# Optimization experiments

Measured on AMD Instinct MI355X. Metric: run time of the kernel, lower is better.

Reference implementation:

```python
import jax, jax.numpy as jnp
import numpy as np

BATCH = 16384
MODEL_DIM = 768
SAE_HIDDEN = 16384
K = 3


def setup_inputs() -> dict:
    key = jax.random.key(0)
    k1, k2, k3, k4, k5 = jax.random.split(key, 5)
    scale_enc = 1.0 / np.sqrt(MODEL_DIM)
    scale_dec = 1.0 / np.sqrt(SAE_HIDDEN)
    return {
        "model_activations": jax.random.normal(k1, (BATCH, MODEL_DIM), jnp.float32),
        "W_enc": jax.random.normal(k2, (SAE_HIDDEN, MODEL_DIM), jnp.float32) * scale_enc,
        "b_enc": jax.random.normal(k3, (SAE_HIDDEN,), jnp.float32) * scale_enc,
        "W_dec": jax.random.normal(k4, (MODEL_DIM, SAE_HIDDEN), jnp.float32) * scale_dec,
        "b_dec": jax.random.normal(k5, (MODEL_DIM,), jnp.float32) * scale_dec,
    }


def reference(model_activations, W_enc, b_enc, W_dec, b_dec):
    # encoder linear: [B, D] @ [D, H] + [H] -> [B, H]
    pre_activations = model_activations @ W_enc.T + b_enc
    # top-k (k=3) per row
    topk_vals, topk_idx = jax.lax.top_k(pre_activations, K)  # [B, K]
    # scatter the k values into a zero tensor (sparse activation)
    B = pre_activations.shape[0]
    rows = jnp.arange(B)[:, None]  # [B, 1]
    sae_activations = jnp.zeros_like(pre_activations).at[rows, topk_idx].set(topk_vals)
    # number of unique live latents across the whole batch (static-shape version of torch.unique)
    live_mask = jnp.zeros((pre_activations.shape[1],), dtype=jnp.bool_).at[topk_idx.reshape(-1)].set(True)
    num_live_latents = jnp.sum(live_mask.astype(jnp.int32))
    # decoder linear: [B, H] @ [H, D] + [D] -> [B, D]
    reconstructed = sae_activations @ W_dec.T + b_dec
    return reconstructed, num_live_latents
```

## Files before the change

kernel.cpp:

```cpp
#include <hip/hip_runtime.h>
#include <cstdint>
#include <cstddef>

#define B_ROWS 16384
#define DIM    768
#define HID    16384
#define BM     256
#define BK     32
#define KT     (DIM / BK)
#define NCB    (HID / BM)

typedef __bf16 bf16x8 __attribute__((ext_vector_type(8)));
typedef float  f32x4  __attribute__((ext_vector_type(4)));
typedef unsigned int   u32;
typedef unsigned short u16;

__device__ __forceinline__ u32 umaxu(u32 a, u32 b) { return a > b ? a : b; }
__device__ __forceinline__ u32 uminu(u32 a, u32 b) { return a < b ? a : b; }

__device__ __forceinline__ u16 f2bf(float f) {
    u32 u = __float_as_uint(f);
    return (u16)((u + 0x7FFFu + ((u >> 16) & 1u)) >> 16);
}

__device__ __forceinline__ u32 pk(float v, int gidx) {
    u32 b = __float_as_uint(v);
    u32 t = b >> 16;
    t ^= (b & 0x80000000u) ? 0xFFFFu : 0x8000u;
    return (t << 16) | (u32)gidx;
}

__device__ __forceinline__ void gll16(const void* g, void* l) {
    __builtin_amdgcn_global_load_lds(
        (const __attribute__((address_space(1))) unsigned int*)g,
        (__attribute__((address_space(3))) unsigned int*)l, 16, 0, 0);
}

__device__ __forceinline__ void merge3(u32& z0, u32& z1, u32& z2,
                                       u32 A0, u32 A1, u32 A2,
                                       u32 B0, u32 B1, u32 B2) {
    const u32 P = uminu(A0, B0), Q = umaxu(A1, B1);
    const u32 R = uminu(A1, B1), S = umaxu(A2, B2);
    z0 = umaxu(A0, B0);
    z1 = umaxu(P, Q);
    z2 = umaxu(umaxu(uminu(P, Q), R), S);
}

__device__ __forceinline__ bool better(float v1, int i1, float v2, int i2) {
    return (v1 > v2) || (v1 == v2 && i1 < i2);
}
__device__ __forceinline__ void ins3(float v, int i,
                                     float& v0, int& i0, float& v1, int& i1,
                                     float& v2, int& i2) {
    if (better(v, i, v2, i2)) {
        v2 = v; i2 = i;
        if (better(v2, i2, v1, i1)) { float tv = v1; int ti = i1; v1 = v2; i1 = i2; v2 = tv; i2 = ti; }
        if (better(v1, i1, v0, i0)) { float tv = v0; int ti = i0; v0 = v1; i0 = i1; v1 = tv; i1 = ti; }
    }
}

__global__ __launch_bounds__(256) void cast_bf16(const float* __restrict__ X,
                                                 const float* __restrict__ W,
                                                 u16* __restrict__ Xb, u16* __restrict__ Wb) {
    const int n4 = (B_ROWS * DIM) / 4;
    for (int i = blockIdx.x * blockDim.x + threadIdx.x; i < n4; i += gridDim.x * blockDim.x) {
        float4 x = ((const float4*)X)[i];
        float4 w = ((const float4*)W)[i];
        ushort4 xo, wo;
        xo.x = f2bf(x.x); xo.y = f2bf(x.y); xo.z = f2bf(x.z); xo.w = f2bf(x.w);
        wo.x = f2bf(w.x); wo.y = f2bf(w.y); wo.z = f2bf(w.z); wo.w = f2bf(w.w);
        ((ushort4*)Xb)[i] = xo;
        ((ushort4*)Wb)[i] = wo;
    }
}

__global__ __launch_bounds__(512, 2) void gemm_screen(const u16* __restrict__ Xb,
                                                      const u16* __restrict__ Wb,
                                                      const float* __restrict__ benc,
                                                      u32* __restrict__ pvpi) {
    __shared__ __align__(16) u16 As[4 * BM * BK];
    __shared__ __align__(16) u16 Bs[4 * BM * BK];

    const int bid = blockIdx.x;
    const int wg = ((bid & 7) << 9) | (bid >> 3);
    const int st = wg >> 8, loc = wg & 255;
    const int rb = ((st >> 2) << 4) | (loc >> 4);
    const int cbk = ((st & 3) << 4) | (loc & 15);
    const int rowBase = rb * BM, colBase = cbk * BM;

    const int tid = threadIdx.x;
    const int wid = tid >> 6, lane = tid & 63;
    const int wm = wid >> 2, wn = wid & 3;
    const int j = lane & 15, g = lane >> 4;

    u32 srcA[2], srcB[2];
#pragma unroll
    for (int q = 0; q < 2; ++q) {
        const int p = q * 512 + tid;
        const int line = p >> 3, slot = p & 7;
        const int c = slot ^ (line & 7);
        const int row = (line << 1) | (c >> 2);
        const int gc = c & 3;
        srcA[q] = (u32)(rowBase + row) * DIM + (u32)gc * 8;
        srcB[q] = (u32)(colBase + row) * DIM + (u32)gc * 8;
    }
    const int lbw = wid * 512;

#define STAGE(T) do { \
    const int rb_ = ((T) & 3) * 8192; \
    const u32 ko_ = (u32)(T) * 32u; \
    gll16(Xb + srcA[0] + ko_, As + rb_ + lbw); \
    gll16(Xb + srcA[1] + ko_, As + rb_ + 4096 + lbw); \
    gll16(Wb + srcB[0] + ko_, Bs + rb_ + lbw); \
    gll16(Wb + srcB[1] + ko_, Bs + rb_ + 4096 + lbw); \
} while (0)

    const int lh = j >> 1;
    const int cg = (j & 1) * 4 + g;
    int aoff[8], boff[4];
#pragma unroll
    for (int m = 0; m < 8; ++m) aoff[m] = (wm * 64 + m * 8 + lh) * 8 + (cg ^ lh);
#pragma unroll
    for (int n = 0; n < 4; ++n) boff[n] = (wn * 32 + n * 8 + lh) * 8 + (cg ^ lh);

    f32x4 acc[8][4];
#pragma unroll
    for (int mt = 0; mt < 8; ++mt)
#pragma unroll
        for (int nt = 0; nt < 4; ++nt) acc[mt][nt] = (f32x4){0.f, 0.f, 0.f, 0.f};

    STAGE(0); STAGE(1); STAGE(2);
    asm volatile("s_waitcnt vmcnt(8)" ::: "memory");
    __builtin_amdgcn_s_barrier();

#pragma unroll 1
    for (int t = 0; t < KT; ++t) {
        if (t + 3 < KT) STAGE(t + 3);

        const bf16x8* Ab = (const bf16x8*)As + (t & 3) * 1024;
        const bf16x8* Bb = (const bf16x8*)Bs + (t & 3) * 1024;
        bf16x8 bF[4], aF[8];
#pragma unroll
        for (int n = 0; n < 4; ++n) bF[n] = Bb[boff[n]];
#pragma unroll
        for (int m = 0; m < 8; ++m) aF[m] = Ab[aoff[m]];

        __builtin_amdgcn_s_setprio(1);
#pragma unroll
        for (int m = 0; m < 8; ++m)
#pragma unroll
            for (int n = 0; n < 4; ++n)
                acc[m][n] = __builtin_amdgcn_mfma_f32_16x16x32_bf16(bF[n], aF[m], acc[m][n], 0, 0, 0);
        __builtin_amdgcn_s_setprio(0);

        if (t + 3 < KT)      asm volatile("s_waitcnt vmcnt(8)" ::: "memory");
        else if (t + 2 < KT) asm volatile("s_waitcnt vmcnt(4)" ::: "memory");
        else if (t + 1 < KT) asm volatile("s_waitcnt vmcnt(0)" ::: "memory");
        if (t + 1 < KT) __builtin_amdgcn_s_barrier();
    }

    __syncthreads();
    u32* sm = (u32*)As;

    float bias[4][4];
#pragma unroll
    for (int nt = 0; nt < 4; ++nt) {
        const float4 b4 = *(const float4*)(benc + colBase + wn * 64 + nt * 16 + g * 4);
        bias[nt][0] = b4.x; bias[nt][1] = b4.y; bias[nt][2] = b4.z; bias[nt][3] = b4.w;
    }
    const int cb0 = colBase + wn * 64 + g * 4;

#pragma unroll
    for (int mt = 0; mt < 8; ++mt) {
        u32 x0 = 0, x1 = 0, x2 = 0;
#pragma unroll
        for (int nt = 0; nt < 4; ++nt) {
#pragma unroll
            for (int reg = 0; reg < 4; ++reg) {
                const u32 k = pk(acc[mt][nt][reg] + bias[nt][reg], cb0 + nt * 16 + reg);
                const u32 t1 = uminu(x0, k), t2 = uminu(x1, k);
                x0 = umaxu(x0, k); x1 = umaxu(x1, t1); x2 = umaxu(x2, t2);
            }
        }
#pragma unroll
        for (int mk = 16; mk <= 32; mk <<= 1) {
            const u32 y0 = (u32)__shfl_xor((int)x0, mk, 64);
            const u32 y1 = (u32)__shfl_xor((int)x1, mk, 64);
            const u32 y2 = (u32)__shfl_xor((int)x2, mk, 64);
            u32 z0, z1, z2;
            merge3(z0, z1, z2, x0, x1, x2, y0, y1, y2);
            x0 = z0; x1 = z1; x2 = z2;
        }
        if (lane < 16) {
            const int row = wm * 128 + mt * 16 + j;
            sm[row * 12 + wn * 3 + 0] = x0;
            sm[row * 12 + wn * 3 + 1] = x1;
            sm[row * 12 + wn * 3 + 2] = x2;
        }
    }
    __syncthreads();
    if (tid < 256) {
        const int row = tid;
        const u32* s = sm + row * 12;
        u32 m0, m1, m2, n0, n1, n2, z0, z1, z2;
        merge3(m0, m1, m2, s[0], s[1], s[2], s[3], s[4], s[5]);
        merge3(n0, n1, n2, s[6], s[7], s[8], s[9], s[10], s[11]);
        merge3(z0, z1, z2, m0, m1, m2, n0, n1, n2);
        const size_t base = ((size_t)(rowBase + row) * NCB + cbk) * 3;
        pvpi[base + 0] = z0; pvpi[base + 1] = z1; pvpi[base + 2] = z2;
    }
#undef STAGE
}

__global__ __launch_bounds__(256) void reduce_recheck(
        const u32* __restrict__ pvpi, const float* __restrict__ X,
        const float* __restrict__ Wenc, const float* __restrict__ benc,
        float* __restrict__ fv, int* __restrict__ fi, int* __restrict__ mask) {
    const int wid = threadIdx.x >> 6, lane = threadIdx.x & 63;
    const int row = blockIdx.x * 4 + wid;

    const u32* p = pvpi + (size_t)row * (NCB * 3);
    u32 k[3];
#pragma unroll
    for (int t = 0; t < 3; t++) k[t] = p[t * 64 + lane];

    u32 cand[16];
#pragma unroll
    for (int it = 0; it < 16; ++it) {
        u32 m = umaxu(umaxu(k[0], k[1]), k[2]);
#pragma unroll
        for (int mk = 1; mk < 64; mk <<= 1) m = umaxu(m, (u32)__shfl_xor((int)m, mk, 64));
        cand[it] = m;
#pragma unroll
        for (int t = 0; t < 3; t++) if (k[t] == m) k[t] = 0;
    }

    const float4* xp = (const float4*)(X + (size_t)row * DIM) + lane * 3;
    const float4 x0 = xp[0], x1 = xp[1], x2 = xp[2];

    float v0 = -INFINITY, v1 = -INFINITY, v2 = -INFINITY;
    int   i0 = 0x7fffffff, i1 = 0x7fffffff, i2 = 0x7fffffff;
#pragma unroll
    for (int it = 0; it < 16; ++it) {
        const int ci = (int)(cand[it] & 0xFFFFu);
        const float4* wq = (const float4*)(Wenc + (size_t)ci * DIM) + lane * 3;
        const float4 w0 = wq[0], w1 = wq[1], w2 = wq[2];
        float s = x0.x * w0.x;
        s = fmaf(x0.y, w0.y, s); s = fmaf(x0.z, w0.z, s); s = fmaf(x0.w, w0.w, s);
        s = fmaf(x1.x, w1.x, s); s = fmaf(x1.y, w1.y, s); s = fmaf(x1.z, w1.z, s);
        s = fmaf(x1.w, w1.w, s); s = fmaf(x2.x, w2.x, s); s = fmaf(x2.y, w2.y, s);
        s = fmaf(x2.z, w2.z, s); s = fmaf(x2.w, w2.w, s);
#pragma unroll
        for (int mk = 1; mk < 64; mk <<= 1) s += __shfl_xor(s, mk, 64);
        const float val = s + benc[ci];
        ins3(val, ci, v0, i0, v1, i1, v2, i2);
    }
    if (lane == 0) {
        fv[row * 3 + 0] = v0; fv[row * 3 + 1] = v1; fv[row * 3 + 2] = v2;
        fi[row * 3 + 0] = i0; fi[row * 3 + 1] = i1; fi[row * 3 + 2] = i2;
        mask[i0] = 1; mask[i1] = 1; mask[i2] = 1;
    }
}

__global__ __launch_bounds__(256) void count_live(const int* __restrict__ mask,
                                                  float* __restrict__ outScalar) {
    __shared__ int sd[256];
    const int tid = threadIdx.x;
    int s = 0;
    for (int i = tid; i < HID; i += 256) s += mask[i];
    sd[tid] = s;
    __syncthreads();
    for (int st = 128; st > 0; st >>= 1) {
        if (tid < st) sd[tid] += sd[tid + st];
        __syncthreads();
    }
    if (tid == 0) outScalar[0] = (float)sd[0];
}

__global__ __launch_bounds__(256) void transpose_wdec(const float* __restrict__ W,
                                                      float* __restrict__ Wt) {
    __shared__ float t[32][33];
    const int bx = blockIdx.x;
    const int by = blockIdx.y;
    const int x = threadIdx.x & 31;
    const int y = threadIdx.x >> 5;
#pragma unroll
    for (int i = 0; i < 4; i++) {
        const int d = by * 32 + y + i * 8;
        t[y + i * 8][x] = W[(size_t)d * HID + bx * 32 + x];
    }
    __syncthreads();
#pragma unroll
    for (int i = 0; i < 4; i++) {
        const int h = bx * 32 + y + i * 8;
        Wt[(size_t)h * DIM + by * 32 + x] = t[x][y + i * 8];
    }
}

__global__ __launch_bounds__(192) void decode_rows(
        const float* __restrict__ fv, const int* __restrict__ fi,
        const float* __restrict__ Wt, const float* __restrict__ bdec,
        float* __restrict__ out) {
    const int row = blockIdx.x;
    const int tid = threadIdx.x;
    const float v0 = fv[row * 3 + 0], v1 = fv[row * 3 + 1], v2 = fv[row * 3 + 2];
    const int   i0 = fi[row * 3 + 0], i1 = fi[row * 3 + 1], i2 = fi[row * 3 + 2];
    const int jj = tid * 4;
    const float4 b  = *(const float4*)(bdec + jj);
    const float4 w0 = *(const float4*)(Wt + (size_t)i0 * DIM + jj);
    const float4 w1 = *(const float4*)(Wt + (size_t)i1 * DIM + jj);
    const float4 w2 = *(const float4*)(Wt + (size_t)i2 * DIM + jj);
    float4 o;
    o.x = b.x + v0 * w0.x + v1 * w1.x + v2 * w2.x;
    o.y = b.y + v0 * w0.y + v1 * w1.y + v2 * w2.y;
    o.z = b.z + v0 * w0.z + v1 * w1.z + v2 * w2.z;
    o.w = b.w + v0 * w0.w + v1 * w1.w + v2 * w2.w;
    *(float4*)(out + (size_t)row * DIM + jj) = o;
}

extern "C" void kernel_launch(void* const* d_in, const int* in_sizes, int n_in,
                              void* d_out, int out_size, void* d_ws, size_t ws_size,
                              hipStream_t stream) {
    const float* X    = (const float*)d_in[0];
    const float* Wenc = (const float*)d_in[1];
    const float* benc = (const float*)d_in[2];
    const float* Wdec = (const float*)d_in[3];
    const float* bdec = (const float*)d_in[4];
    float* out = (float*)d_out;

    char* ws = (char*)d_ws;
    u16*   Xb   = (u16*)ws;
    u16*   Wb   = (u16*)(ws + 25165824);
    float* Wt   = (float*)ws;
    u32*   pvpi = (u32*)(ws + 50331648);
    float* fv   = (float*)(ws + 62914560);
    int*   fi   = (int*)(ws + 63111168);
    int*   mask = (int*)(ws + 63307776);

    hipMemsetAsync(mask, 0, HID * sizeof(int), stream);

    cast_bf16<<<3072, 256, 0, stream>>>(X, Wenc, Xb, Wb);
    gemm_screen<<<4096, 512, 0, stream>>>(Xb, Wb, benc, pvpi);
    reduce_recheck<<<B_ROWS / 4, 256, 0, stream>>>(pvpi, X, Wenc, benc, fv, fi, mask);
    count_live<<<1, 256, 0, stream>>>(mask, out + (size_t)B_ROWS * DIM);
    transpose_wdec<<<dim3(HID / 32, DIM / 32), 256, 0, stream>>>(Wdec, Wt);
    decode_rows<<<B_ROWS, 192, 0, stream>>>(fv, fi, Wt, bdec, out);
}
```

Baseline: 879.0 us.

## Double-buffer LDS fragment reads and unroll the K loop by four

The encoder GEMM main loop is unrolled four ways with static LDS slot indices. The A/B fragments for the next tile are read from shared memory into a second register set while the current tile's MFMAs issue, so LDS read latency overlaps with matrix math. The vmcnt waits are retuned so only one tile is prefetched ahead. This doubles the fragment registers and puts ring-slot wraparound into hand-written code that must stay consistent with the barriers.

```diff
diff --git a/kernel.cpp b/kernel.cpp
--- a/kernel.cpp
+++ b/kernel.cpp
@@ -106,22 +106,40 @@
     }
     const int lbw = wid * 512;
 
-#define STAGE(T) do { \
-    const int rb_ = ((T) & 3) * 8192; \
-    const u32 ko_ = (u32)(T) * 32u; \
-    gll16(Xb + srcA[0] + ko_, As + rb_ + lbw); \
-    gll16(Xb + srcA[1] + ko_, As + rb_ + 4096 + lbw); \
-    gll16(Wb + srcB[0] + ko_, Bs + rb_ + lbw); \
-    gll16(Wb + srcB[1] + ko_, Bs + rb_ + 4096 + lbw); \
+#define STAGE(TT, SL) do { \
+    const u32 ko_ = (u32)(TT) * 32u; \
+    gll16(Xb + srcA[0] + ko_, As + (SL) * 8192 + lbw); \
+    gll16(Xb + srcA[1] + ko_, As + (SL) * 8192 + 4096 + lbw); \
+    gll16(Wb + srcB[0] + ko_, Bs + (SL) * 8192 + lbw); \
+    gll16(Wb + srcB[1] + ko_, Bs + (SL) * 8192 + 4096 + lbw); \
 } while (0)
 
     const int lh = j >> 1;
     const int cg = (j & 1) * 4 + g;
-    int aoff[8], boff[4];
-#pragma unroll
-    for (int m = 0; m < 8; ++m) aoff[m] = (wm * 64 + m * 8 + lh) * 8 + (cg ^ lh);
-#pragma unroll
-    for (int n = 0; n < 4; ++n) boff[n] = (wn * 32 + n * 8 + lh) * 8 + (cg ^ lh);
+    const int abase = wm * 512 + lh * 8 + (cg ^ lh);
+    const int bbase = wn * 256 + lh * 8 + (cg ^ lh);
+
+    const bf16x8* As8 = (const bf16x8*)As;
+    const bf16x8* Bs8 = (const bf16x8*)Bs;
+
+#define READS(SL, AF, BF) do { \
+    _Pragma("unroll") for (int n_ = 0; n_ < 4; ++n_) BF[n_] = Bs8[bbase + (SL) * 1024 + n_ * 64]; \
+    _Pragma("unroll") for (int m_ = 0; m_ < 8; ++m_) AF[m_] = As8[abase + (SL) * 1024 + m_ * 64]; \
+} while (0)
+
+#define MFMAS(AF, BF) do { \
+    __builtin_amdgcn_s_setprio(1); \
+    _Pragma("unroll") for (int m_ = 0; m_ < 8; ++m_) \
+    _Pragma("unroll") for (int n_ = 0; n_ < 4; ++n_) \
+        acc[m_][n_] = __builtin_amdgcn_mfma_f32_16x16x32_bf16(BF[n_], AF[m_], acc[m_][n_], 0, 0, 0); \
+    __builtin_amdgcn_s_setprio(0); \
+} while (0)
+
+#define ENDTILE(T) do { \
+    if ((T) + 3 < KT)      asm volatile("s_waitcnt vmcnt(4)" ::: "memory"); \
+    else if ((T) + 2 < KT) asm volatile("s_waitcnt vmcnt(0)" ::: "memory"); \
+    if ((T) + 1 < KT) __builtin_amdgcn_s_barrier(); \
+} while (0)
 
     f32x4 acc[8][4];
 #pragma unroll
@@ -129,34 +147,31 @@
 #pragma unroll
         for (int nt = 0; nt < 4; ++nt) acc[mt][nt] = (f32x4){0.f, 0.f, 0.f, 0.f};
 
-    STAGE(0); STAGE(1); STAGE(2);
-    asm volatile("s_waitcnt vmcnt(8)" ::: "memory");
+    STAGE(0, 0); STAGE(1, 1); STAGE(2, 2);
+    asm volatile("s_waitcnt vmcnt(4)" ::: "memory");
     __builtin_amdgcn_s_barrier();
 
+    bf16x8 aE[8], bE[4], aO[8], bO[4];
+    READS(0, aE, bE);
+
 #pragma unroll 1
-    for (int t = 0; t < KT; ++t) {
-        if (t + 3 < KT) STAGE(t + 3);
-
-        const bf16x8* Ab = (const bf16x8*)As + (t & 3) * 1024;
-        const bf16x8* Bb = (const bf16x8*)Bs + (t & 3) * 1024;
-        bf16x8 bF[4], aF[8];
-#pragma unroll
-        for (int n = 0; n < 4; ++n) bF[n] = Bb[boff[n]];
-#pragma unroll
-        for (int m = 0; m < 8; ++m) aF[m] = Ab[aoff[m]];
-
-        __builtin_amdgcn_s_setprio(1);
-#pragma unroll
-        for (int m = 0; m < 8; ++m)
-#pragma unroll
-            for (int n = 0; n < 4; ++n)
-                acc[m][n] = __builtin_amdgcn_mfma_f32_16x16x32_bf16(bF[n], aF[m], acc[m][n], 0, 0, 0);
-        __builtin_amdgcn_s_setprio(0);
-
-        if (t + 3 < KT)      asm volatile("s_waitcnt vmcnt(8)" ::: "memory");
-        else if (t + 2 < KT) asm volatile("s_waitcnt vmcnt(4)" ::: "memory");
-        else if (t + 1 < KT) asm volatile("s_waitcnt vmcnt(0)" ::: "memory");
-        if (t + 1 < KT) __builtin_amdgcn_s_barrier();
+    for (int tt = 0; tt < KT; tt += 4) {
+        if (tt + 3 < KT) STAGE(tt + 3, 3);
+        READS(1, aO, bO);
+        MFMAS(aE, bE);
+        ENDTILE(tt);
+        if (tt + 4 < KT) STAGE(tt + 4, 0);
+        READS(2, aE, bE);
+        MFMAS(aO, bO);
+        ENDTILE(tt + 1);
+        if (tt + 5 < KT) STAGE(tt + 5, 1);
+        READS(3, aO, bO);
+        MFMAS(aE, bE);
+        ENDTILE(tt + 2);
+        if (tt + 6 < KT) STAGE(tt + 6, 2);
+        if (tt + 4 < KT) READS(0, aE, bE);
+        MFMAS(aO, bO);
+        ENDTILE(tt + 3);
     }
 
     __syncthreads();
@@ -210,6 +225,9 @@
         pvpi[base + 0] = z0; pvpi[base + 1] = z1; pvpi[base + 2] = z2;
     }
 #undef STAGE
+#undef READS
+#undef MFMAS
+#undef ENDTILE
 }
 
 __global__ __launch_bounds__(256) void reduce_recheck(
```

Result: slower. 1.437 ms (+63.5%).
